# Kernel tuning notes

Hardware: AMD Instinct MI355X
Metric: run time of the kernel (lower is better)

Reference implementation:

```python
import jax, jax.numpy as jnp
import numpy as np

B, T, D_IN, D_SAE, K = 256, 8, 768, 8192, 32


def setup_inputs() -> dict:
    key = jax.random.key(0)
    k1, k2, k3 = jax.random.split(key, 3)
    x = jax.random.normal(k1, (B, T, D_IN), dtype=jnp.float32)
    # kaiming_uniform: bound = sqrt(6 / fan_in), fan_in = prod of trailing dims
    bound_e = float(np.sqrt(6.0 / (D_SAE * D_IN)))
    W_enc = jax.random.uniform(k2, (T, D_SAE, D_IN), jnp.float32, -bound_e, bound_e)
    bound_d = float(np.sqrt(6.0 / (D_IN * D_SAE)))
    W_dec = jax.random.uniform(k3, (T, D_IN, D_SAE), jnp.float32, -bound_d, bound_d)
    # decoder column normalization (norm over d_in axis), as in _normalize_decoder
    norms = jnp.clip(jnp.linalg.norm(W_dec, axis=1, keepdims=True), 1e-8)
    W_dec = W_dec / norms
    b_enc = jnp.zeros((T, D_SAE), jnp.float32)
    b_dec = jnp.zeros((T, D_IN), jnp.float32)
    return {"x": x, "W_enc": W_enc, "b_enc": b_enc, "W_dec": W_dec,
            "b_dec": b_dec, "k": K}


def reference(x, W_enc, b_enc, W_dec, b_dec, k):
    # x: (B, T, d_in)
    x_c = x - b_dec[None]                                   # (B, T, d)
    pre = jnp.einsum('btd,thd->bth', x_c, W_enc) + b_enc[None]  # (B, T, h)
    bt = pre.shape[0] * pre.shape[1]
    pre_flat = pre.reshape(bt, -1)
    topk_vals, topk_idx = jax.lax.top_k(pre_flat, k)        # (BT, k)
    rows = jnp.arange(bt)[:, None]
    u_flat = jnp.zeros_like(pre_flat).at[rows, topk_idx].set(jax.nn.relu(topk_vals))
    u = u_flat.reshape(pre.shape)                            # (B, T, h)
    x_hat = jnp.einsum('bth,tdh->btd', u, W_dec) + b_dec[None]
    recon_loss = jnp.mean(jnp.sum((x_hat - x) ** 2, axis=-1))
    return recon_loss, x_hat, u
```

## Files before the change

### kernel.cpp

```cpp
#include <hip/hip_runtime.h>
#include <cstdint>
#include <cstddef>

constexpr int B_SZ  = 256;
constexpr int T_SZ  = 8;
constexpr int DIN   = 768;
constexpr int DSAE  = 8192;
constexpr int KSEL  = 32;
constexpr int NROWS = B_SZ * T_SZ;
constexpr int CAND_CAP = 64;
constexpr int RCAP  = 32;
constexpr float EPS_W = 3.2e-4f;

constexpr size_t XC_SZ    = (size_t)NROWS * DIN;
constexpr size_t OFF_XC   = 0;
constexpr size_t OFF_XCB  = OFF_XC + XC_SZ;
constexpr size_t XCB_WORDS = XC_SZ / 2;
constexpr size_t OFF_SIDX = OFF_XCB + XCB_WORDS;
constexpr size_t OFF_SVAL = OFF_SIDX + (size_t)NROWS * KSEL;
constexpr size_t OFF_WT   = OFF_SVAL + (size_t)NROWS * KSEL;
constexpr size_t WT_WORDS = (size_t)T_SZ * DSAE * DIN / 2;
constexpr size_t WS_FAST_WORDS = OFF_WT + WT_WORDS;

typedef short bf16x8 __attribute__((ext_vector_type(8)));
typedef float f32x4  __attribute__((ext_vector_type(4)));

__device__ inline unsigned rne1(float x) {
  unsigned u = __float_as_uint(x);
  return (u + 0x7FFFu + ((u >> 16) & 1u)) >> 16;
}
__device__ inline float bf16tof(unsigned short v) {
  return __uint_as_float((unsigned)v << 16);
}
__device__ inline unsigned packtr(float a, float b) {
  return (__float_as_uint(a) >> 16) | (__float_as_uint(b) & 0xFFFF0000u);
}

__device__ inline void gload_lds16(const void* g, void* l) {
  __builtin_amdgcn_global_load_lds(
      (const __attribute__((address_space(1))) void*)g,
      (__attribute__((address_space(3))) void*)l, 16, 0, 0);
}

__global__ void k_zero(float* p) { *p = 0.f; }

__global__ __launch_bounds__(256) void k_xc(const float* __restrict__ x,
                                            const float* __restrict__ bdec,
                                            float* __restrict__ xc,
                                            unsigned short* __restrict__ xcb) {
  int n = NROWS * DIN;
  for (int i = blockIdx.x * 256 + threadIdx.x; i < n; i += gridDim.x * 256) {
    int d = i % DIN;
    int t = (i / DIN) & (T_SZ - 1);
    float v = x[i] - bdec[t * DIN + d];
    xc[i] = v;
    xcb[i] = (unsigned short)rne1(v);
  }
}

__global__ __launch_bounds__(256, 4) void k_encoder(const unsigned short* __restrict__ xcb,
                                                    const float* __restrict__ Wenc,
                                                    const float* __restrict__ benc,
                                                    float* __restrict__ pre) {
  const int t  = blockIdx.y;
  const int n0 = blockIdx.x * 64;
  constexpr int NS = DIN / 32;
  __shared__ __align__(16) float Bs[2][64 * 32];
  const int tid = threadIdx.x;

  int gRow[2], gCol[2], ldsL[2];
#pragma unroll
  for (int i = 0; i < 2; ++i) {
    int L = i * 4096 + tid * 16;
    int G = L ^ (((L >> 7) & 7) << 4);
    gRow[i] = G >> 7;
    gCol[i] = (G & 127) >> 2;
    ldsL[i] = L;
  }
  auto STAGE = [&](int buf, int s) {
#pragma unroll
    for (int i = 0; i < 2; ++i) {
      const float* src = Wenc + ((size_t)t * DSAE + n0 + gRow[i]) * DIN + s * 32 + gCol[i];
      gload_lds16(src, (char*)&Bs[buf][0] + ldsL[i]);
    }
  };

  const int wm = tid >> 6, lane = tid & 63;
  const int l15 = lane & 15, kc = lane >> 4;
  const unsigned short* aBase =
      xcb + ((size_t)(wm * 64 + l15) * T_SZ + t) * DIN + kc * 8;
  constexpr size_t A_MI = (size_t)16 * T_SZ * DIN;
  int bOff0[4], bOff1[4];
#pragma unroll
  for (int ni = 0; ni < 4; ++ni) {
    int row = ni * 16 + l15;
    int P = row * 128 + kc * 32;
    int sw = (row & 7) << 4;
    bOff0[ni] = P ^ sw;
    bOff1[ni] = (P + 16) ^ sw;
  }

  f32x4 acc[4][4] = {};
  STAGE(0, 0);
  __syncthreads();
  int cur = 0;
  for (int s = 0; s < NS; ++s) {
    if (s + 1 < NS) STAGE(cur ^ 1, s + 1);
    bf16x8 a[4];
#pragma unroll
    for (int mi = 0; mi < 4; ++mi)
      a[mi] = *(const bf16x8*)(aBase + s * 32 + mi * A_MI);
    bf16x8 bf[4];
#pragma unroll
    for (int ni = 0; ni < 4; ++ni) {
      f32x4 f0 = *(const f32x4*)((const char*)&Bs[cur][0] + bOff0[ni]);
      f32x4 f1 = *(const f32x4*)((const char*)&Bs[cur][0] + bOff1[ni]);
      union { uint32_t u[4]; bf16x8 h; } cv;
      cv.u[0] = packtr(f0.x, f0.y); cv.u[1] = packtr(f0.z, f0.w);
      cv.u[2] = packtr(f1.x, f1.y); cv.u[3] = packtr(f1.z, f1.w);
      bf[ni] = cv.h;
    }
#pragma unroll
    for (int mi = 0; mi < 4; ++mi)
#pragma unroll
      for (int ni = 0; ni < 4; ++ni)
        acc[mi][ni] = __builtin_amdgcn_mfma_f32_16x16x32_bf16(
            a[mi], bf[ni], acc[mi][ni], 0, 0, 0);
    __syncthreads();
    cur ^= 1;
  }

#pragma unroll
  for (int ni = 0; ni < 4; ++ni) {
    const int col = n0 + ni * 16 + l15;
    const float bias = benc[(size_t)t * DSAE + col];
#pragma unroll
    for (int mi = 0; mi < 4; ++mi) {
      const int rbase = wm * 64 + mi * 16 + kc * 4;
#pragma unroll
      for (int j = 0; j < 4; ++j)
        pre[((size_t)(rbase + j) * T_SZ + t) * DSAE + col] = acc[mi][ni][j] + bias;
    }
  }
}

__global__ __launch_bounds__(256) void k_select(const float* __restrict__ xc,
                                                const float* __restrict__ Wenc,
                                                const float* __restrict__ benc,
                                                float* u,
                                                int* __restrict__ sel_idx,
                                                float* __restrict__ sel_val) {
  const int r = blockIdx.x, t = r & (T_SZ - 1);
  __shared__ float sp[DSAE];
  __shared__ float redf[4], redf2[4];
  __shared__ int   redi[4];
  __shared__ float cv[CAND_CAP]; __shared__ int ci[CAND_CAP];
  __shared__ float sv[CAND_CAP]; __shared__ int si[CAND_CAP];
  __shared__ float rv[RCAP];     __shared__ int ri[RCAP];
  __shared__ double rd[RCAP];
  __shared__ double xd[DIN];
  __shared__ int   s_n, s_nR, s_A, s_nW;
  const int tid = threadIdx.x, lane = tid & 63, w = tid >> 6;
  float* urow = u + (size_t)r * DSAE;

  float s1 = 0.f, s2 = 0.f;
  for (int sgm = 0; sgm < DSAE / 256; ++sgm) {
    float v = urow[tid + sgm * 256];
    sp[tid + sgm * 256] = v;
    s1 += v; s2 = fmaf(v, v, s2);
  }
  for (int off = 32; off; off >>= 1) {
    s1 += __shfl_down(s1, off); s2 += __shfl_down(s2, off);
  }
  if (lane == 0) { redf[w] = s1; redf2[w] = s2; }
  __syncthreads();
  const float mean = (redf[0] + redf[1] + redf[2] + redf[3]) * (1.f / DSAE);
  const float var  = (redf2[0] + redf2[1] + redf2[2] + redf2[3]) * (1.f / DSAE) - mean * mean;
  const float sd   = sqrtf(fmaxf(var, 1e-20f));

  auto countGE = [&](float th) -> int {
    int c = 0;
#pragma unroll
    for (int sgm = 0; sgm < DSAE / 256; ++sgm)
      c += (sp[tid + sgm * 256] >= th) ? 1 : 0;
    for (int off = 32; off; off >>= 1) c += __shfl_down(c, off);
    __syncthreads();
    if (lane == 0) redi[w] = c;
    __syncthreads();
    return redi[0] + redi[1] + redi[2] + redi[3];
  };

  float tlo = mean + 2.0f * sd, thi = mean + 3.5f * sd;
  for (int it = 0; it < 8 && countGE(tlo) < KSEL; ++it) tlo -= sd;
  float th = mean + 2.52f * sd;
  int c = countGE(th);
  for (int it = 0; it < 24 && (c < KSEL || c > CAND_CAP); ++it) {
    if (c > CAND_CAP) tlo = th; else thi = th;
    th = 0.5f * (tlo + thi);
    c = countGE(th);
  }
  if (c < KSEL) { th = tlo; c = countGE(th); }

  if (tid == 0) s_n = 0;
  __syncthreads();
  for (int sgm = 0; sgm < DSAE / 256; ++sgm) {
    int i = tid + sgm * 256;
    float v = sp[i];
    if (v >= th) {
      int p = atomicAdd(&s_n, 1);
      if (p < CAND_CAP) { cv[p] = v; ci[p] = i; }
    }
  }
  __syncthreads();
  const int n = s_n < CAND_CAP ? s_n : CAND_CAP;

  if (tid < n) {
    float v = cv[tid]; int id = ci[tid];
    int rk = 0;
    for (int j = 0; j < n; ++j) {
      float vj = cv[j];
      rk += (vj > v || (vj == v && ci[j] < id)) ? 1 : 0;
    }
    sv[rk] = v; si[rk] = id;
  }
  __syncthreads();

  const float v32 = sv[KSEL - 1];
  const float wlo = v32 - EPS_W, whi = v32 + EPS_W;
  if (tid == 0) {
    int A = 0;
    while (A < KSEL - 1 && sv[A] > whi) ++A;
    s_A = A;
    int e = A;
    while (e < n && sv[e] >= wlo) ++e;
    s_nW = e - A;
  }
  __syncthreads();
  const int A  = s_A;
  const int nW = s_nW < RCAP ? s_nW : RCAP;
  if (tid < nW) { rv[tid] = sv[A + tid]; ri[tid] = si[A + tid]; }
  if (tid == 0) s_nR = nW;
  __syncthreads();
  if (th > wlo) {
    for (int sgm = 0; sgm < DSAE / 256; ++sgm) {
      int i = tid + sgm * 256;
      float v = sp[i];
      if (v >= wlo && v < th) {
        int p = atomicAdd(&s_nR, 1);
        if (p < RCAP) { rv[p] = v; ri[p] = i; }
      }
    }
  }
  __syncthreads();
  const int nR = s_nR < RCAP ? s_nR : RCAP;

  if (nR >= 2) {
    for (int i = tid; i < DIN; i += 256) xd[i] = (double)xc[(size_t)r * DIN + i];
    __syncthreads();
    for (int j = w; j < nR; j += 4) {
      const int h = ri[j];
      const float* wrow = Wenc + ((size_t)t * DSAE + h) * DIN;
      double s = 0.0;
#pragma unroll
      for (int ss = 0; ss < DIN / 64; ++ss)
        s += xd[lane + 64 * ss] * (double)wrow[lane + 64 * ss];
      for (int off = 32; off; off >>= 1) s += __shfl_down(s, off);
      if (lane == 0) rd[j] = s + (double)benc[(size_t)t * DSAE + h];
    }
  } else if (nR == 1) {
    if (tid == 0) rd[0] = (double)rv[0];
  }
  __syncthreads();

  for (int sgm = 0; sgm < DSAE / 256; ++sgm) urow[tid + sgm * 256] = 0.f;
  __syncthreads();

  if (tid < A) {
    float val = fmaxf(sv[tid], 0.f);
    urow[si[tid]] = val;
    sel_idx[(size_t)r * KSEL + tid] = si[tid];
    sel_val[(size_t)r * KSEL + tid] = val;
  }
  const int need = KSEL - A;
  if (tid < nR) {
    double v = rd[tid]; int id = ri[tid];
    int rk = 0;
    for (int j = 0; j < nR; ++j) {
      double vj = rd[j];
      rk += (vj > v || (vj == v && ri[j] < id)) ? 1 : 0;
    }
    if (rk < need) {
      float val = fmaxf((float)v, 0.f);
      urow[id] = val;
      sel_idx[(size_t)r * KSEL + A + rk] = id;
      sel_val[(size_t)r * KSEL + A + rk] = val;
    }
  }
}

__global__ __launch_bounds__(256) void k_transpose(const float* __restrict__ W,
                                                   unsigned short* __restrict__ Wt) {
  __shared__ float s[32][33];
  const int t  = blockIdx.z;
  const int h0 = blockIdx.x * 32;
  const int d0 = blockIdx.y * 32;
  const int c  = threadIdx.x & 31, rr = threadIdx.x >> 5;
#pragma unroll
  for (int q = 0; q < 4; ++q) {
    int d = d0 + rr + q * 8;
    s[rr + q * 8][c] = W[((size_t)t * DIN + d) * DSAE + h0 + c];
  }
  __syncthreads();
#pragma unroll
  for (int q = 0; q < 4; ++q) {
    int h = h0 + rr + q * 8;
    Wt[((size_t)t * DSAE + h) * DIN + d0 + c] = (unsigned short)rne1(s[c][rr + q * 8]);
  }
}

template <bool TRANSPOSED>
__global__ __launch_bounds__(256) void k_decoder(const void* __restrict__ Wd_,
                                                 const float* __restrict__ x,
                                                 const float* __restrict__ bdec,
                                                 const int* __restrict__ sel_idx,
                                                 const float* __restrict__ sel_val,
                                                 float* __restrict__ xhat,
                                                 float* __restrict__ loss) {
  const int r = blockIdx.x, t = r & (T_SZ - 1);
  __shared__ int   si[KSEL];
  __shared__ float sv[KSEL];
  __shared__ float rbuf[4];
  const int tid = threadIdx.x;
  if (tid < KSEL) {
    si[tid] = sel_idx[(size_t)r * KSEL + tid] & (DSAE - 1);
    sv[tid] = sel_val[(size_t)r * KSEL + tid];
  }
  __syncthreads();

  float acc[3];
#pragma unroll
  for (int i = 0; i < 3; ++i) acc[i] = bdec[(size_t)t * DIN + tid + 256 * i];
#pragma unroll 4
  for (int j = 0; j < KSEL; ++j) {
    const int h = si[j];
    const float v = sv[j];
    if (TRANSPOSED) {
      const unsigned short* wrow =
          (const unsigned short*)Wd_ + ((size_t)t * DSAE + h) * DIN;
#pragma unroll
      for (int i = 0; i < 3; ++i)
        acc[i] = fmaf(v, bf16tof(wrow[tid + 256 * i]), acc[i]);
    } else {
      const float* Wd = (const float*)Wd_;
#pragma unroll
      for (int i = 0; i < 3; ++i)
        acc[i] = fmaf(v, Wd[((size_t)t * DIN + tid + 256 * i) * DSAE + h], acc[i]);
    }
  }
  float sq = 0.f;
#pragma unroll
  for (int i = 0; i < 3; ++i) {
    const int d = tid + 256 * i;
    const float xv = x[(size_t)r * DIN + d];
    xhat[(size_t)r * DIN + d] = acc[i];
    const float e = acc[i] - xv;
    sq = fmaf(e, e, sq);
  }
  for (int off = 32; off; off >>= 1) sq += __shfl_down(sq, off);
  if ((tid & 63) == 0) rbuf[tid >> 6] = sq;
  __syncthreads();
  if (tid == 0)
    atomicAdd(loss, (rbuf[0] + rbuf[1] + rbuf[2] + rbuf[3]) * (1.0f / NROWS));
}

extern "C" void kernel_launch(void* const* d_in, const int* in_sizes, int n_in,
                              void* d_out, int out_size, void* d_ws, size_t ws_size,
                              hipStream_t stream) {
  const float* x    = (const float*)d_in[0];
  const float* Wenc = (const float*)d_in[1];
  const float* benc = (const float*)d_in[2];
  const float* Wdec = (const float*)d_in[3];
  const float* bdec = (const float*)d_in[4];

  float* out  = (float*)d_out;
  float* loss = out;
  float* xhat = out + 1;
  float* u    = out + 1 + (size_t)NROWS * DIN;

  float*          wsf  = (float*)d_ws;
  float*          xc   = wsf + OFF_XC;
  unsigned short* xcb  = (unsigned short*)(wsf + OFF_XCB);
  int*            sidx = (int*)(wsf + OFF_SIDX);
  float*          sval = wsf + OFF_SVAL;
  unsigned short* wt   = (unsigned short*)(wsf + OFF_WT);
  const bool fast = ws_size >= WS_FAST_WORDS * sizeof(float);

  k_zero<<<1, 1, 0, stream>>>(loss);
  k_xc<<<1536, 256, 0, stream>>>(x, bdec, xc, xcb);
  k_encoder<<<dim3(DSAE / 64, T_SZ), 256, 0, stream>>>(xcb, Wenc, benc, u);
  k_select<<<NROWS, 256, 0, stream>>>(xc, Wenc, benc, u, sidx, sval);
  if (fast) {
    k_transpose<<<dim3(DSAE / 32, DIN / 32, T_SZ), 256, 0, stream>>>(Wdec, wt);
    k_decoder<true><<<NROWS, 256, 0, stream>>>(wt, x, bdec, sidx, sval, xhat, loss);
  } else {
    k_decoder<false><<<NROWS, 256, 0, stream>>>(Wdec, x, bdec, sidx, sval, xhat, loss);
  }
}
```

Baseline: 259.1 us.

## Load encoder weights directly from global memory instead of LDS double-buffering

The encoder GEMM drops its LDS double-buffered staging of W_enc (global_load_lds with XOR swizzle and per-step barriers). Each wave now reads its B fragments straight from global memory, converts them to bf16 in registers and feeds the MFMAs, with the k-loop unrolled by four. This removes the LDS round trip and the __syncthreads per k-step. The cost is that the four waves of a block each fetch the same weight tile themselves, relying on L1/L2 for reuse, and global latency is no longer hidden by explicit prefetch.

```diff
diff --git a/kernel.cpp b/kernel.cpp
--- a/kernel.cpp
+++ b/kernel.cpp
@@ -34,12 +34,6 @@
 }
 __device__ inline unsigned packtr(float a, float b) {
   return (__float_as_uint(a) >> 16) | (__float_as_uint(b) & 0xFFFF0000u);
-}
-
-__device__ inline void gload_lds16(const void* g, void* l) {
-  __builtin_amdgcn_global_load_lds(
-      (const __attribute__((address_space(1))) void*)g,
-      (__attribute__((address_space(3))) void*)l, 16, 0, 0);
 }
 
 __global__ void k_zero(float* p) { *p = 0.f; }
@@ -65,69 +59,38 @@
   const int t  = blockIdx.y;
   const int n0 = blockIdx.x * 64;
   constexpr int NS = DIN / 32;
-  __shared__ __align__(16) float Bs[2][64 * 32];
   const int tid = threadIdx.x;
-
-  int gRow[2], gCol[2], ldsL[2];
-#pragma unroll
-  for (int i = 0; i < 2; ++i) {
-    int L = i * 4096 + tid * 16;
-    int G = L ^ (((L >> 7) & 7) << 4);
-    gRow[i] = G >> 7;
-    gCol[i] = (G & 127) >> 2;
-    ldsL[i] = L;
-  }
-  auto STAGE = [&](int buf, int s) {
-#pragma unroll
-    for (int i = 0; i < 2; ++i) {
-      const float* src = Wenc + ((size_t)t * DSAE + n0 + gRow[i]) * DIN + s * 32 + gCol[i];
-      gload_lds16(src, (char*)&Bs[buf][0] + ldsL[i]);
-    }
-  };
-
   const int wm = tid >> 6, lane = tid & 63;
   const int l15 = lane & 15, kc = lane >> 4;
+
   const unsigned short* aBase =
       xcb + ((size_t)(wm * 64 + l15) * T_SZ + t) * DIN + kc * 8;
   constexpr size_t A_MI = (size_t)16 * T_SZ * DIN;
-  int bOff0[4], bOff1[4];
-#pragma unroll
-  for (int ni = 0; ni < 4; ++ni) {
-    int row = ni * 16 + l15;
-    int P = row * 128 + kc * 32;
-    int sw = (row & 7) << 4;
-    bOff0[ni] = P ^ sw;
-    bOff1[ni] = (P + 16) ^ sw;
-  }
+
+  const char* bPtr[4];
+#pragma unroll
+  for (int ni = 0; ni < 4; ++ni)
+    bPtr[ni] = (const char*)(Wenc + ((size_t)t * DSAE + n0 + ni * 16 + l15) * DIN) + kc * 32;
 
   f32x4 acc[4][4] = {};
-  STAGE(0, 0);
-  __syncthreads();
-  int cur = 0;
+#pragma unroll 4
   for (int s = 0; s < NS; ++s) {
-    if (s + 1 < NS) STAGE(cur ^ 1, s + 1);
     bf16x8 a[4];
 #pragma unroll
     for (int mi = 0; mi < 4; ++mi)
       a[mi] = *(const bf16x8*)(aBase + s * 32 + mi * A_MI);
-    bf16x8 bf[4];
 #pragma unroll
     for (int ni = 0; ni < 4; ++ni) {
-      f32x4 f0 = *(const f32x4*)((const char*)&Bs[cur][0] + bOff0[ni]);
-      f32x4 f1 = *(const f32x4*)((const char*)&Bs[cur][0] + bOff1[ni]);
+      f32x4 f0 = *(const f32x4*)(bPtr[ni] + s * 128);
+      f32x4 f1 = *(const f32x4*)(bPtr[ni] + s * 128 + 16);
       union { uint32_t u[4]; bf16x8 h; } cv;
       cv.u[0] = packtr(f0.x, f0.y); cv.u[1] = packtr(f0.z, f0.w);
       cv.u[2] = packtr(f1.x, f1.y); cv.u[3] = packtr(f1.z, f1.w);
-      bf[ni] = cv.h;
-    }
-#pragma unroll
-    for (int mi = 0; mi < 4; ++mi)
-#pragma unroll
-      for (int ni = 0; ni < 4; ++ni)
+#pragma unroll
+      for (int mi = 0; mi < 4; ++mi)
         acc[mi][ni] = __builtin_amdgcn_mfma_f32_16x16x32_bf16(
-            a[mi], bf[ni], acc[mi][ni], 0, 0, 0);
-    __syncthreads();
-    cur ^= 1;
+            a[mi], cv.h, acc[mi][ni], 0, 0, 0);
+    }
   }
 
 #pragma unroll
```

Result: slower. 327.8 us (+26.5%).

## Deepen encoder GEMM pipeline to four LDS stages with persistent two-tile blocks

Applied to the files above, without the earlier changes.

The encoder GEMM now uses four LDS buffers and prefetches two k-steps ahead, with explicit vmcnt waits and raw barriers instead of a double buffer synchronised with __syncthreads. The A-operand registers are also double-buffered one step ahead. The grid shrinks to 512 blocks, each processing two output tiles, and launch bounds drop to 2 waves per EU. The aim is to hide global-load latency for W_enc and xcb, at the cost of more LDS and registers per block and fragile hand-counted wait counts.

```diff
diff --git a/kernel.cpp b/kernel.cpp
--- a/kernel.cpp
+++ b/kernel.cpp
@@ -58,15 +58,15 @@
   }
 }
 
-__global__ __launch_bounds__(256, 4) void k_encoder(const unsigned short* __restrict__ xcb,
+__global__ __launch_bounds__(256, 2) void k_encoder(const unsigned short* __restrict__ xcb,
                                                     const float* __restrict__ Wenc,
                                                     const float* __restrict__ benc,
                                                     float* __restrict__ pre) {
-  const int t  = blockIdx.y;
-  const int n0 = blockIdx.x * 64;
   constexpr int NS = DIN / 32;
-  __shared__ __align__(16) float Bs[2][64 * 32];
+  __shared__ __align__(16) float Bs[4][64 * 32];
   const int tid = threadIdx.x;
+  const int wm = tid >> 6, lane = tid & 63;
+  const int l15 = lane & 15, kc = lane >> 4;
 
   int gRow[2], gCol[2], ldsL[2];
 #pragma unroll
@@ -77,19 +77,6 @@
     gCol[i] = (G & 127) >> 2;
     ldsL[i] = L;
   }
-  auto STAGE = [&](int buf, int s) {
-#pragma unroll
-    for (int i = 0; i < 2; ++i) {
-      const float* src = Wenc + ((size_t)t * DSAE + n0 + gRow[i]) * DIN + s * 32 + gCol[i];
-      gload_lds16(src, (char*)&Bs[buf][0] + ldsL[i]);
-    }
-  };
-
-  const int wm = tid >> 6, lane = tid & 63;
-  const int l15 = lane & 15, kc = lane >> 4;
-  const unsigned short* aBase =
-      xcb + ((size_t)(wm * 64 + l15) * T_SZ + t) * DIN + kc * 8;
-  constexpr size_t A_MI = (size_t)16 * T_SZ * DIN;
   int bOff0[4], bOff1[4];
 #pragma unroll
   for (int ni = 0; ni < 4; ++ni) {
@@ -99,48 +86,91 @@
     bOff0[ni] = P ^ sw;
     bOff1[ni] = (P + 16) ^ sw;
   }
-
-  f32x4 acc[4][4] = {};
-  STAGE(0, 0);
-  __syncthreads();
-  int cur = 0;
-  for (int s = 0; s < NS; ++s) {
-    if (s + 1 < NS) STAGE(cur ^ 1, s + 1);
-    bf16x8 a[4];
-#pragma unroll
-    for (int mi = 0; mi < 4; ++mi)
-      a[mi] = *(const bf16x8*)(aBase + s * 32 + mi * A_MI);
-    bf16x8 bf[4];
+  constexpr size_t A_MI = (size_t)16 * T_SZ * DIN;
+
+  for (int tile = 0; tile < 2; ++tile) {
+    const int tileId = blockIdx.x + tile * 512;
+    const int t  = tileId >> 7;
+    const int n0 = (tileId & 127) * 64;
+
+    const float* bG = Wenc + ((size_t)t * DSAE + n0) * DIN;
+    const unsigned short* aBase =
+        xcb + ((size_t)(wm * 64 + l15) * T_SZ + t) * DIN + kc * 8;
+
+    auto STAGE = [&](int buf, int s) {
+#pragma unroll
+      for (int i = 0; i < 2; ++i)
+        gload_lds16(bG + (size_t)gRow[i] * DIN + s * 32 + gCol[i],
+                    (char*)&Bs[0][0] + buf * 8192 + ldsL[i]);
+    };
+
+    f32x4 acc[4][4] = {};
+    bf16x8 aA[4], aB[4];
+
+    STAGE(0, 0);
+#pragma unroll
+    for (int mi = 0; mi < 4; ++mi) aA[mi] = *(const bf16x8*)(aBase + mi * A_MI);
+    STAGE(1, 1);
+
+#define ENC_W6 asm volatile("s_waitcnt vmcnt(6)" ::: "memory")
+#define ENC_W4 asm volatile("s_waitcnt vmcnt(4)" ::: "memory")
+#define ENC_W0 asm volatile("s_waitcnt vmcnt(0)" ::: "memory")
+#define ENC_STEP(u, PFB, PFA, WAITOP) do {                                   \
+    if (PFB) STAGE(((u) + 2) & 3, s0 + (u) + 2);                             \
+    if (PFA) {                                                               \
+      const unsigned short* ap = aBase + (size_t)(s0 + (u) + 1) * 32;        \
+      _Pragma("unroll")                                                      \
+      for (int mi = 0; mi < 4; ++mi) {                                       \
+        bf16x8 v = *(const bf16x8*)(ap + mi * A_MI);                         \
+        if ((u) % 2 == 0) aB[mi] = v; else aA[mi] = v;                       \
+      }                                                                      \
+    }                                                                        \
+    __builtin_amdgcn_sched_barrier(0);                                       \
+    WAITOP;                                                                  \
+    __builtin_amdgcn_s_barrier();                                            \
+    __builtin_amdgcn_sched_barrier(0);                                       \
+    {                                                                        \
+      const char* bb = (const char*)&Bs[0][0] + ((u) & 3) * 8192;            \
+      _Pragma("unroll")                                                      \
+      for (int ni = 0; ni < 4; ++ni) {                                       \
+        f32x4 f0 = *(const f32x4*)(bb + bOff0[ni]);                          \
+        f32x4 f1 = *(const f32x4*)(bb + bOff1[ni]);                          \
+        union { uint32_t w[4]; bf16x8 h; } cv;                               \
+        cv.w[0] = packtr(f0.x, f0.y); cv.w[1] = packtr(f0.z, f0.w);          \
+        cv.w[2] = packtr(f1.x, f1.y); cv.w[3] = packtr(f1.z, f1.w);          \
+        _Pragma("unroll")                                                    \
+        for (int mi = 0; mi < 4; ++mi)                                       \
+          acc[mi][ni] = __builtin_amdgcn_mfma_f32_16x16x32_bf16(             \
+              ((u) % 2 == 0) ? aA[mi] : aB[mi], cv.h, acc[mi][ni], 0, 0, 0); \
+      }                                                                      \
+    }                                                                        \
+  } while (0)
+
+    int s0 = 0;
+    for (int g = 0; g < 5; ++g, s0 += 4) {
+      ENC_STEP(0, true, true, ENC_W6); ENC_STEP(1, true, true, ENC_W6);
+      ENC_STEP(2, true, true, ENC_W6); ENC_STEP(3, true, true, ENC_W6);
+    }
+    ENC_STEP(0, true, true, ENC_W6);  ENC_STEP(1, true, true, ENC_W6);
+    ENC_STEP(2, false, true, ENC_W4); ENC_STEP(3, false, false, ENC_W0);
+#undef ENC_STEP
+#undef ENC_W6
+#undef ENC_W4
+#undef ENC_W0
+
 #pragma unroll
     for (int ni = 0; ni < 4; ++ni) {
-      f32x4 f0 = *(const f32x4*)((const char*)&Bs[cur][0] + bOff0[ni]);
-      f32x4 f1 = *(const f32x4*)((const char*)&Bs[cur][0] + bOff1[ni]);
-      union { uint32_t u[4]; bf16x8 h; } cv;
-      cv.u[0] = packtr(f0.x, f0.y); cv.u[1] = packtr(f0.z, f0.w);
-      cv.u[2] = packtr(f1.x, f1.y); cv.u[3] = packtr(f1.z, f1.w);
-      bf[ni] = cv.h;
-    }
-#pragma unroll
-    for (int mi = 0; mi < 4; ++mi)
-#pragma unroll
-      for (int ni = 0; ni < 4; ++ni)
-        acc[mi][ni] = __builtin_amdgcn_mfma_f32_16x16x32_bf16(
-            a[mi], bf[ni], acc[mi][ni], 0, 0, 0);
-    __syncthreads();
-    cur ^= 1;
-  }
-
-#pragma unroll
-  for (int ni = 0; ni < 4; ++ni) {
-    const int col = n0 + ni * 16 + l15;
-    const float bias = benc[(size_t)t * DSAE + col];
-#pragma unroll
-    for (int mi = 0; mi < 4; ++mi) {
-      const int rbase = wm * 64 + mi * 16 + kc * 4;
-#pragma unroll
-      for (int j = 0; j < 4; ++j)
-        pre[((size_t)(rbase + j) * T_SZ + t) * DSAE + col] = acc[mi][ni][j] + bias;
-    }
+      const int col = n0 + ni * 16 + l15;
+      const float bias = benc[(size_t)t * DSAE + col];
+#pragma unroll
+      for (int mi = 0; mi < 4; ++mi) {
+        const int rbase = wm * 64 + mi * 16 + kc * 4;
+#pragma unroll
+        for (int j = 0; j < 4; ++j)
+          pre[((size_t)(rbase + j) * T_SZ + t) * DSAE + col] = acc[mi][ni][j] + bias;
+      }
+    }
+    if (tile == 0) __syncthreads();
   }
 }
 
@@ -397,7 +427,7 @@
 
   k_zero<<<1, 1, 0, stream>>>(loss);
   k_xc<<<1536, 256, 0, stream>>>(x, bdec, xc, xcb);
-  k_encoder<<<dim3(DSAE / 64, T_SZ), 256, 0, stream>>>(xcb, Wenc, benc, u);
+  k_encoder<<<512, 256, 0, stream>>>(xcb, Wenc, benc, u);
   k_select<<<NROWS, 256, 0, stream>>>(xc, Wenc, benc, u, sidx, sval);
   if (fast) {
     k_transpose<<<dim3(DSAE / 32, DIN / 32, T_SZ), 256, 0, stream>>>(Wdec, wt);
```

New measurement: 263.5 us. Within noise of the previous version (+1.7%).
